# Optimization experiments

Hardware: AMD Instinct MI355X
Metric: run time of the kernel (lower is better)

## Reference

```python
import jax, jax.numpy as jnp
import numpy as np

D_MODEL = 1024
N_HEADS = 16
D_K = 64
D_V = 64
NEG = -1e9
EPS = 1e-6


def setup_inputs() -> dict:
    key = jax.random.key(0)
    ks = jax.random.split(key, 7)
    B, L = 8, 1024
    X = jax.random.normal(ks[0], (B, L, D_MODEL), dtype=jnp.float32)
    attn_mask = jax.random.randint(ks[1], (B, 1, L, L), 0, 2) == 1  # True = masked
    s = 1.0 / np.sqrt(D_MODEL)
    W_Q = jax.random.normal(ks[2], (D_MODEL, N_HEADS * D_K), dtype=jnp.float32) * s
    W_K = jax.random.normal(ks[3], (D_MODEL, N_HEADS * D_K), dtype=jnp.float32) * s
    W_V = jax.random.normal(ks[4], (D_MODEL, N_HEADS * D_V), dtype=jnp.float32) * s
    W_O = jax.random.normal(ks[5], (N_HEADS * D_V, D_MODEL), dtype=jnp.float32) * (1.0 / np.sqrt(N_HEADS * D_V))
    gamma = jnp.ones((D_MODEL,), dtype=jnp.float32)
    beta = jnp.zeros((D_MODEL,), dtype=jnp.float32)
    return {"X": X, "attn_mask": attn_mask, "W_Q": W_Q, "W_K": W_K,
            "W_V": W_V, "W_O": W_O, "gamma": gamma, "beta": beta}


def _layer_norm(x, gamma, beta):
    mu = jnp.mean(x, axis=-1, keepdims=True)
    var = jnp.mean(jnp.square(x - mu), axis=-1, keepdims=True)
    return (x - mu) * jax.lax.rsqrt(var + EPS) * gamma + beta


def reference(X, attn_mask, W_Q, W_K, W_V, W_O, gamma, beta):
    B, L, _ = X.shape
    # project and split heads: [B, H, L, d]
    Q = (X @ W_Q).reshape(B, L, N_HEADS, D_K).transpose(0, 2, 1, 3)
    K = (X @ W_K).reshape(B, L, N_HEADS, D_K).transpose(0, 2, 1, 3)
    V = (X @ W_V).reshape(B, L, N_HEADS, D_V).transpose(0, 2, 1, 3)
    scale = 1.0 / np.sqrt(D_K)
    scores = jnp.einsum('bhqd,bhkd->bhqk', Q, K) * scale  # [B,H,L,L]
    scores = jnp.where(attn_mask, NEG, scores)
    attn = jax.nn.softmax(scores, axis=-1)
    context = jnp.einsum('bhqk,bhkd->bhqd', attn, V)  # [B,H,L,d_v]
    context = context.transpose(0, 2, 1, 3).reshape(B, L, N_HEADS * D_V)
    output = context @ W_O
    return _layer_norm(output + X, gamma, beta), attn
```

## Files before the change

kernel.cpp:

```cpp
#include <hip/hip_runtime.h>
#include <cstdint>


#define WS_XB   0u
#define WS_WT   16777216u
#define WS_WOT  (WS_WT + 6291456u)
#define WS_M8   (WS_WOT + 2097152u)
#define WS_Q    (WS_M8 + 8388608u)
#define WS_K    (WS_Q + 16777216u)
#define WS_V    (WS_K + 16777216u)

typedef short v8s __attribute__((ext_vector_type(8)));
typedef float v4f __attribute__((ext_vector_type(4)));

__device__ __forceinline__ short bf16rn(float f) {
  uint32_t u = __builtin_bit_cast(uint32_t, f);
  u += 0x7fffu + ((u >> 16) & 1u);
  return (short)(u >> 16);
}
__device__ __forceinline__ uint32_t bfpack(float a, float b) {
  return (uint32_t)(uint16_t)bf16rn(a) | ((uint32_t)(uint16_t)bf16rn(b) << 16);
}
__device__ __forceinline__ float bf2f(uint16_t h) {
  uint32_t u = ((uint32_t)h) << 16;
  return __builtin_bit_cast(float, u);
}
__device__ __forceinline__ v4f mfma16(v8s a, v8s b, v4f c) {
  return __builtin_amdgcn_mfma_f32_16x16x32_bf16(a, b, c, 0, 0, 0);
}
__device__ __forceinline__ void gload16(const short* g, short* l) {
  __builtin_amdgcn_global_load_lds(
      (const __attribute__((address_space(1))) unsigned int*)g,
      (__attribute__((address_space(3))) unsigned int*)l, 16, 0, 0);
}

__global__ void k_cvt_x(const float* __restrict__ X, short* __restrict__ Xb) {
  int i = (blockIdx.x * 256 + threadIdx.x) * 4;
  float4 v = *(const float4*)(X + i);
  short4 o;
  o.x = bf16rn(v.x); o.y = bf16rn(v.y); o.z = bf16rn(v.z); o.w = bf16rn(v.w);
  *(short4*)(Xb + i) = o;
}

__global__ void k_tw(const float* __restrict__ WQ, const float* __restrict__ WK,
                     const float* __restrict__ WV, const float* __restrict__ WO,
                     short* __restrict__ Wt, short* __restrict__ WOt) {
  __shared__ float tile[32][33];
  int k0 = blockIdx.x * 32, n0 = blockIdx.y * 32;
  int tx = threadIdx.x, ty = threadIdx.y;
  const float* src; short* dst; int nloc, drow;
  if (n0 < 3072) {
    int wsel = n0 >> 10;
    src = wsel == 0 ? WQ : (wsel == 1 ? WK : WV);
    nloc = n0 & 1023; dst = Wt; drow = n0;
  } else {
    src = WO; nloc = n0 - 3072; dst = WOt; drow = n0 - 3072;
  }
#pragma unroll
  for (int i = 0; i < 4; ++i)
    tile[ty + 8 * i][tx] = src[(size_t)(k0 + ty + 8 * i) * 1024 + nloc + tx];
  __syncthreads();
#pragma unroll
  for (int i = 0; i < 4; ++i)
    dst[(size_t)(drow + ty + 8 * i) * 1024 + k0 + tx] = bf16rn(tile[tx][ty + 8 * i]);
}

__global__ void k_msk(const int* __restrict__ M, uint32_t* __restrict__ Mb) {
  int i = blockIdx.x * 256 + threadIdx.x;
  unsigned long long bal = __ballot(M[i] != 0);
  int lane = threadIdx.x & 63;
  if (lane == 0)       Mb[i >> 5] = (uint32_t)bal;
  else if (lane == 32) Mb[i >> 5] = (uint32_t)(bal >> 32);
}

template <int MODE>
__global__ __launch_bounds__(256) void k_gemm(const short* __restrict__ A,
                                              const short* __restrict__ Bt,
                                              short* __restrict__ Q, short* __restrict__ Kp,
                                              short* __restrict__ V,
                                              const float* __restrict__ Xres,
                                              float* __restrict__ Y) {
  __shared__ short As[128 * 32];
  __shared__ short Bs[128 * 32];
  const int nwg = gridDim.x * gridDim.y;
  const int id = blockIdx.y * gridDim.x + blockIdx.x;
  const int swz = (id & 7) * (nwg >> 3) + (id >> 3);
  const int bx = swz % gridDim.x, by = swz / gridDim.x;
  const int m0 = by * 128, n0 = bx * 128;
  const int t = threadIdx.x, w = t >> 6, lane = t & 63, col = lane & 15, quad = lane >> 4;
  const int wm = w >> 1, wn = w & 1;
  const v4f vz = {0.f, 0.f, 0.f, 0.f};
  v4f acc[4][4];
#pragma unroll
  for (int i = 0; i < 4; ++i)
#pragma unroll
    for (int j = 0; j < 4; ++j) acc[i][j] = vz;

  const int srow = lane >> 2, sseg = lane & 3;
  const short* ga = A + (size_t)(m0 + w * 32 + srow) * 1024 + sseg * 8;
  const short* gb = Bt + (size_t)(n0 + w * 32 + srow) * 1024 + sseg * 8;
  short* la = As + (w * 32) * 32;
  short* lb = Bs + (w * 32) * 32;

  for (int kc = 0; kc < 32; ++kc) {
    __syncthreads();
    gload16(ga + kc * 32, la);
    gload16(ga + kc * 32 + 16 * 1024, la + 16 * 32);
    gload16(gb + kc * 32, lb);
    gload16(gb + kc * 32 + 16 * 1024, lb + 16 * 32);
    __syncthreads();
    v8s af[4], bf[4];
#pragma unroll
    for (int i = 0; i < 4; ++i) {
      af[i] = *(const v8s*)(As + (wm * 64 + i * 16 + col) * 32 + quad * 8);
      bf[i] = *(const v8s*)(Bs + (wn * 64 + i * 16 + col) * 32 + quad * 8);
    }
#pragma unroll
    for (int mi = 0; mi < 4; ++mi)
#pragma unroll
      for (int ni = 0; ni < 4; ++ni)
        acc[mi][ni] = mfma16(af[mi], bf[ni], acc[mi][ni]);
  }

  if (MODE == 0) {
    const int which = n0 >> 10;
    if (which == 2) {
#pragma unroll
      for (int mi = 0; mi < 4; ++mi)
#pragma unroll
        for (int ni = 0; ni < 4; ++ni) {
          int n = n0 + wn * 64 + ni * 16 + col;
          int h = (n >> 6) & 15, d = n & 63;
          int mbase = m0 + wm * 64 + mi * 16 + quad * 4;
          int b = mbase >> 10, l = mbase & 1023;
          short4 pk;
          pk.x = bf16rn(acc[mi][ni][0]); pk.y = bf16rn(acc[mi][ni][1]);
          pk.z = bf16rn(acc[mi][ni][2]); pk.w = bf16rn(acc[mi][ni][3]);
          *(short4*)(V + ((size_t)((b * 16 + h) * 64 + d)) * 1024 + l) = pk;
        }
    } else {
      short* dst = which == 0 ? Q : Kp;
      const float qs = which == 0 ? 0.125f : 1.0f;
#pragma unroll
      for (int mi = 0; mi < 4; ++mi)
#pragma unroll
        for (int ni = 0; ni < 4; ++ni) {
          int n = n0 + wn * 64 + ni * 16 + col;
          int h = (n >> 6) & 15, d = n & 63;
          int mbase = m0 + wm * 64 + mi * 16 + quad * 4;
#pragma unroll
          for (int rg = 0; rg < 4; ++rg) {
            int m = mbase + rg, b = m >> 10, l = m & 1023;
            dst[((size_t)((b * 16 + h) * 1024 + l)) * 64 + d] = bf16rn(acc[mi][ni][rg] * qs);
          }
        }
    }
  } else {
#pragma unroll
    for (int mi = 0; mi < 4; ++mi)
#pragma unroll
      for (int ni = 0; ni < 4; ++ni) {
        int n = n0 + wn * 64 + ni * 16 + col;
        int mbase = m0 + wm * 64 + mi * 16 + quad * 4;
#pragma unroll
        for (int rg = 0; rg < 4; ++rg) {
          int m = mbase + rg;
          Y[(size_t)m * 1024 + n] = acc[mi][ni][rg] + Xres[(size_t)m * 1024 + n];
        }
      }
  }
}

__global__ __launch_bounds__(256) void k_attn(const short* __restrict__ Qb,
                                              const short* __restrict__ Kb,
                                              const short* __restrict__ Vt,
                                              const uint32_t* __restrict__ Mb,
                                              float* __restrict__ attn,
                                              short* __restrict__ ctxb) {
  __shared__ short Pb[32 * 136];
  __shared__ float red[4][32];
  __shared__ float fin[32];

  const int lid = blockIdx.y * 32 + blockIdx.x;
  const int swz = (lid & 7) * 512 + (lid >> 3);
  const int bh = swz >> 5, q0 = (swz & 31) * 32, b = bh >> 4, h = bh & 15;
  const int t = threadIdx.x, w = t >> 6, lane = t & 63, col = lane & 15, quad = lane >> 4;
  const v4f vz = {0.f, 0.f, 0.f, 0.f};

  v8s qf[2][2];
#pragma unroll
  for (int qt = 0; qt < 2; ++qt)
#pragma unroll
    for (int dh2 = 0; dh2 < 2; ++dh2)
      qf[qt][dh2] = *(const v8s*)(Qb + ((size_t)bh * 1024 + q0 + qt * 16 + col) * 64 + dh2 * 32 + quad * 8);

  const size_t kvbase = (size_t)bh * 1024;
  const short* gkw = Kb + (kvbase + w * 32 + col) * 64 + quad * 8;
  const uint32_t* mrow0 = Mb + ((size_t)(b * 1024 + q0 + col)) * 32 + w;
  const uint32_t* mrow1 = mrow0 + 16 * 32;

  uint32_t pun[8][2][2][2];
  float lr[2] = {0.f, 0.f};

#pragma unroll
  for (int s = 0; s < 8; ++s) {
    uint32_t mu0 = mrow0[s * 4], mu1 = mrow1[s * 4];
#pragma unroll
    for (int kt = 0; kt < 2; ++kt) {
      const short* grow = gkw + (s * 128 + kt * 16) * 64;
      v8s a0 = *(const v8s*)(grow);
      v8s a1 = *(const v8s*)(grow + 32);
#pragma unroll
      for (int qt = 0; qt < 2; ++qt) {
        uint32_t mu = qt ? mu1 : mu0;
        v4f c = mfma16(a0, qf[qt][0], vz);
        c = mfma16(a1, qf[qt][1], c);
        const int sh = kt * 16 + quad * 4;
        float e0 = ((mu >> (sh + 0)) & 1u) ? 0.f : __expf(c[0]);
        float e1 = ((mu >> (sh + 1)) & 1u) ? 0.f : __expf(c[1]);
        float e2 = ((mu >> (sh + 2)) & 1u) ? 0.f : __expf(c[2]);
        float e3 = ((mu >> (sh + 3)) & 1u) ? 0.f : __expf(c[3]);
        lr[qt] += (e0 + e1) + (e2 + e3);
        pun[s][kt][qt][0] = bfpack(e0, e1);
        pun[s][kt][qt][1] = bfpack(e2, e3);
      }
    }
  }

#pragma unroll
  for (int qt = 0; qt < 2; ++qt) {
    float es = lr[qt];
    es += __shfl_xor(es, 16);
    es += __shfl_xor(es, 32);
    if (quad == 0) red[w][qt * 16 + col] = es;
  }
  __syncthreads();
  if (t < 32) {
    float Lx = red[0][t] + red[1][t] + red[2][t] + red[3][t];
    fin[t] = Lx > 0.f ? 1.f / Lx : 0.f;
  }
  __syncthreads();
  float Rq[2];
  Rq[0] = fin[col]; Rq[1] = fin[16 + col];

  const int qh = w & 1, dh = w >> 1;
  v4f ctx[2] = {vz, vz};

  float* arow0 = attn + ((size_t)bh * 1024 + q0 + col) * 1024 + w * 32 + quad * 4;
  float* arow1 = arow0 + (size_t)16 * 1024;
  short* pbr0 = Pb + col * 136 + w * 32 + quad * 4;
  short* pbr1 = Pb + (16 + col) * 136 + w * 32 + quad * 4;
#pragma unroll
  for (int s = 0; s < 8; ++s) {
#pragma unroll
    for (int kt = 0; kt < 2; ++kt) {
#pragma unroll
      for (int qt = 0; qt < 2; ++qt) {
        uint32_t u01 = pun[s][kt][qt][0], u23 = pun[s][kt][qt][1];
        float rq = qt ? Rq[1] : Rq[0];
        float f0 = bf2f((uint16_t)u01) * rq, f1 = bf2f((uint16_t)(u01 >> 16)) * rq;
        float f2 = bf2f((uint16_t)u23) * rq, f3 = bf2f((uint16_t)(u23 >> 16)) * rq;
        float4 o = {f0, f1, f2, f3};
        *(float4*)((qt ? arow1 : arow0) + s * 128 + kt * 16) = o;
        short* pb = (qt ? pbr1 : pbr0) + kt * 16;
        *(uint32_t*)pb = bfpack(f0, f1);
        *(uint32_t*)(pb + 2) = bfpack(f2, f3);
      }
    }
    __syncthreads();
#pragma unroll
    for (int kc = 0; kc < 128; kc += 32) {
      v8s pa = *(const v8s*)(Pb + (qh * 16 + col) * 136 + kc + quad * 8);
#pragma unroll
      for (int dt = 0; dt < 2; ++dt) {
        int d = dh * 32 + dt * 16 + col;
        v8s vb = *(const v8s*)(Vt + ((size_t)bh * 64 + d) * 1024 + s * 128 + kc + quad * 8);
        ctx[dt] = mfma16(pa, vb, ctx[dt]);
      }
    }
    __syncthreads();
  }
#pragma unroll
  for (int dt = 0; dt < 2; ++dt)
#pragma unroll
    for (int rg = 0; rg < 4; ++rg) {
      int q = q0 + qh * 16 + quad * 4 + rg;
      int d = dh * 32 + dt * 16 + col;
      ctxb[((size_t)(b * 1024 + q)) * 1024 + h * 64 + d] = bf16rn(ctx[dt][rg]);
    }
}

__global__ __launch_bounds__(256) void k_ln(const float* __restrict__ Y,
                                            const float* __restrict__ g,
                                            const float* __restrict__ be,
                                            float* __restrict__ out) {
  __shared__ float sred[4];
  const int row = blockIdx.x, t = threadIdx.x, w = t >> 6, lane = t & 63;
  const float4 v = *(const float4*)(Y + (size_t)row * 1024 + t * 4);
  float sum = v.x + v.y + v.z + v.w;
#pragma unroll
  for (int o = 32; o > 0; o >>= 1) sum += __shfl_down(sum, o);
  if (lane == 0) sred[w] = sum;
  __syncthreads();
  float mu = (sred[0] + sred[1] + sred[2] + sred[3]) * (1.f / 1024.f);
  float dx = v.x - mu, dy = v.y - mu, dz = v.z - mu, dw = v.w - mu;
  float sq = dx * dx + dy * dy + dz * dz + dw * dw;
#pragma unroll
  for (int o = 32; o > 0; o >>= 1) sq += __shfl_down(sq, o);
  __syncthreads();
  if (lane == 0) sred[w] = sq;
  __syncthreads();
  float var = (sred[0] + sred[1] + sred[2] + sred[3]) * (1.f / 1024.f);
  float rs = rsqrtf(var + 1e-6f);
  float4 gg = *(const float4*)(g + t * 4), bb = *(const float4*)(be + t * 4);
  float4 o4;
  o4.x = dx * rs * gg.x + bb.x;
  o4.y = dy * rs * gg.y + bb.y;
  o4.z = dz * rs * gg.z + bb.z;
  o4.w = dw * rs * gg.w + bb.w;
  *(float4*)(out + (size_t)row * 1024 + t * 4) = o4;
}

extern "C" void kernel_launch(void* const* d_in, const int* in_sizes, int n_in,
                              void* d_out, int out_size, void* d_ws, size_t ws_size,
                              hipStream_t stream) {
  const float* X  = (const float*)d_in[0];
  const int*   Mi = (const int*)d_in[1];
  const float* WQ = (const float*)d_in[2];
  const float* WK = (const float*)d_in[3];
  const float* WV = (const float*)d_in[4];
  const float* WO = (const float*)d_in[5];
  const float* g  = (const float*)d_in[6];
  const float* be = (const float*)d_in[7];

  char* ws = (char*)d_ws;
  short*    Xb  = (short*)(ws + WS_XB);
  short*    Wt  = (short*)(ws + WS_WT);
  short*    WOt = (short*)(ws + WS_WOT);
  uint32_t* Mb  = (uint32_t*)(ws + WS_M8);
  short*    Qb  = (short*)(ws + WS_Q);
  short*    Kb  = (short*)(ws + WS_K);
  short*    Vtb = (short*)(ws + WS_V);
  short*    Ctx = Xb;
  float*    Y   = (float*)(ws + WS_Q);

  float* out0 = (float*)d_out;
  float* attn = out0 + (size_t)8 * 1024 * 1024;

  k_cvt_x<<<8192, 256, 0, stream>>>(X, Xb);
  k_tw<<<dim3(32, 128), dim3(32, 8), 0, stream>>>(WQ, WK, WV, WO, Wt, WOt);
  k_msk<<<32768, 256, 0, stream>>>(Mi, Mb);
  k_gemm<0><<<dim3(24, 64), 256, 0, stream>>>(Xb, Wt, Qb, Kb, Vtb, nullptr, nullptr);
  k_attn<<<dim3(32, 128), 256, 0, stream>>>(Qb, Kb, Vtb, Mb, attn, Ctx);
  k_gemm<1><<<dim3(8, 64), 256, 0, stream>>>(Ctx, WOt, nullptr, nullptr, nullptr, X, Y);
  k_ln<<<8192, 256, 0, stream>>>(Y, g, be, out0);
}
```

Measured before the change: 969.3 us.

## Stage K tiles through LDS with register prefetch and merge prep kernels

In the attention kernel, K tiles are now loaded cooperatively into padded shared memory, and the next tile is prefetched into registers while the current one is being computed. Mask words are hoisted into registers up front, and s_setprio brackets the MFMA sections. The X conversion and mask packing kernels are merged into one launch to save a launch and let them overlap. The cost is extra LDS use, two barriers per stage, and more register pressure that could lower occupancy.

Measured after the change: 983.6 us. About the same (+1.5%).

```diff
diff --git a/kernel.cpp b/kernel.cpp
--- a/kernel.cpp
+++ b/kernel.cpp
@@ -34,12 +34,22 @@
       (__attribute__((address_space(3))) unsigned int*)l, 16, 0, 0);
 }
 
-__global__ void k_cvt_x(const float* __restrict__ X, short* __restrict__ Xb) {
-  int i = (blockIdx.x * 256 + threadIdx.x) * 4;
-  float4 v = *(const float4*)(X + i);
-  short4 o;
-  o.x = bf16rn(v.x); o.y = bf16rn(v.y); o.z = bf16rn(v.z); o.w = bf16rn(v.w);
-  *(short4*)(Xb + i) = o;
+__global__ void k_prep(const float* __restrict__ X, short* __restrict__ Xb,
+                       const int* __restrict__ M, uint32_t* __restrict__ Mb) {
+  int bid = blockIdx.x;
+  if (bid < 8192) {
+    int i = (bid * 256 + threadIdx.x) * 4;
+    float4 v = *(const float4*)(X + i);
+    short4 o;
+    o.x = bf16rn(v.x); o.y = bf16rn(v.y); o.z = bf16rn(v.z); o.w = bf16rn(v.w);
+    *(short4*)(Xb + i) = o;
+  } else {
+    int i = (bid - 8192) * 256 + threadIdx.x;
+    unsigned long long bal = __ballot(M[i] != 0);
+    int lane = threadIdx.x & 63;
+    if (lane == 0)       Mb[i >> 5] = (uint32_t)bal;
+    else if (lane == 32) Mb[i >> 5] = (uint32_t)(bal >> 32);
+  }
 }
 
 __global__ void k_tw(const float* __restrict__ WQ, const float* __restrict__ WK,
@@ -63,14 +73,6 @@
 #pragma unroll
   for (int i = 0; i < 4; ++i)
     dst[(size_t)(drow + ty + 8 * i) * 1024 + k0 + tx] = bf16rn(tile[tx][ty + 8 * i]);
-}
-
-__global__ void k_msk(const int* __restrict__ M, uint32_t* __restrict__ Mb) {
-  int i = blockIdx.x * 256 + threadIdx.x;
-  unsigned long long bal = __ballot(M[i] != 0);
-  int lane = threadIdx.x & 63;
-  if (lane == 0)       Mb[i >> 5] = (uint32_t)bal;
-  else if (lane == 32) Mb[i >> 5] = (uint32_t)(bal >> 32);
 }
 
 template <int MODE>
@@ -177,6 +179,7 @@
                                               const uint32_t* __restrict__ Mb,
                                               float* __restrict__ attn,
                                               short* __restrict__ ctxb) {
+  __shared__ short Ks[128 * 72];
   __shared__ short Pb[32 * 136];
   __shared__ float red[4][32];
   __shared__ float fin[32];
@@ -195,24 +198,43 @@
       qf[qt][dh2] = *(const v8s*)(Qb + ((size_t)bh * 1024 + q0 + qt * 16 + col) * 64 + dh2 * 32 + quad * 8);
 
   const size_t kvbase = (size_t)bh * 1024;
-  const short* gkw = Kb + (kvbase + w * 32 + col) * 64 + quad * 8;
   const uint32_t* mrow0 = Mb + ((size_t)(b * 1024 + q0 + col)) * 32 + w;
   const uint32_t* mrow1 = mrow0 + 16 * 32;
+  uint32_t mk[2][8];
+#pragma unroll
+  for (int s = 0; s < 8; ++s) { mk[0][s] = mrow0[s * 4]; mk[1][s] = mrow1[s * 4]; }
+
+  const int r = t >> 1, sg = t & 1;
+  const short* gk0 = Kb + (kvbase + r) * 64 + sg * 32;
+  short* lk = Ks + r * 72 + sg * 32;
 
   uint32_t pun[8][2][2][2];
   float lr[2] = {0.f, 0.f};
 
+  {
+    int4 c0 = ((const int4*)gk0)[0], c1 = ((const int4*)gk0)[1];
+    int4 c2 = ((const int4*)gk0)[2], c3 = ((const int4*)gk0)[3];
+    ((int4*)lk)[0] = c0; ((int4*)lk)[1] = c1; ((int4*)lk)[2] = c2; ((int4*)lk)[3] = c3;
+  }
+  __syncthreads();
+
 #pragma unroll
   for (int s = 0; s < 8; ++s) {
-    uint32_t mu0 = mrow0[s * 4], mu1 = mrow1[s * 4];
+    int4 n0, n1, n2, n3;
+    if (s < 7) {
+      const short* gk = gk0 + (size_t)(s + 1) * 128 * 64;
+      n0 = ((const int4*)gk)[0]; n1 = ((const int4*)gk)[1];
+      n2 = ((const int4*)gk)[2]; n3 = ((const int4*)gk)[3];
+    }
+    __builtin_amdgcn_s_setprio(1);
 #pragma unroll
     for (int kt = 0; kt < 2; ++kt) {
-      const short* grow = gkw + (s * 128 + kt * 16) * 64;
-      v8s a0 = *(const v8s*)(grow);
-      v8s a1 = *(const v8s*)(grow + 32);
+      int kr0 = w * 32 + kt * 16;
+      v8s a0 = *(const v8s*)(Ks + (kr0 + col) * 72 + quad * 8);
+      v8s a1 = *(const v8s*)(Ks + (kr0 + col) * 72 + 32 + quad * 8);
 #pragma unroll
       for (int qt = 0; qt < 2; ++qt) {
-        uint32_t mu = qt ? mu1 : mu0;
+        uint32_t mu = mk[qt][s];
         v4f c = mfma16(a0, qf[qt][0], vz);
         c = mfma16(a1, qf[qt][1], c);
         const int sh = kt * 16 + quad * 4;
@@ -225,6 +247,13 @@
         pun[s][kt][qt][1] = bfpack(e2, e3);
       }
     }
+    __builtin_amdgcn_s_setprio(0);
+    __syncthreads();
+    if (s < 7) {
+      ((int4*)lk)[0] = n0; ((int4*)lk)[1] = n1;
+      ((int4*)lk)[2] = n2; ((int4*)lk)[3] = n3;
+    }
+    __syncthreads();
   }
 
 #pragma unroll
@@ -268,6 +297,7 @@
       }
     }
     __syncthreads();
+    __builtin_amdgcn_s_setprio(1);
 #pragma unroll
     for (int kc = 0; kc < 128; kc += 32) {
       v8s pa = *(const v8s*)(Pb + (qh * 16 + col) * 136 + kc + quad * 8);
@@ -278,6 +308,7 @@
         ctx[dt] = mfma16(pa, vb, ctx[dt]);
       }
     }
+    __builtin_amdgcn_s_setprio(0);
     __syncthreads();
   }
 #pragma unroll
@@ -347,9 +378,8 @@
   float* out0 = (float*)d_out;
   float* attn = out0 + (size_t)8 * 1024 * 1024;
 
-  k_cvt_x<<<8192, 256, 0, stream>>>(X, Xb);
+  k_prep<<<40960, 256, 0, stream>>>(X, Xb, Mi, Mb);
   k_tw<<<dim3(32, 128), dim3(32, 8), 0, stream>>>(WQ, WK, WV, WO, Wt, WOt);
-  k_msk<<<32768, 256, 0, stream>>>(Mi, Mb);
   k_gemm<0><<<dim3(24, 64), 256, 0, stream>>>(Xb, Wt, Qb, Kb, Vtb, nullptr, nullptr);
   k_attn<<<dim3(32, 128), 256, 0, stream>>>(Qb, Kb, Vtb, Mb, attn, Ctx);
   k_gemm<1><<<dim3(8, 64), 256, 0, stream>>>(Ctx, WOt, nullptr, nullptr, nullptr, X, Y);
```
